# Kernel tuning notes

Hardware: AMD Instinct MI355X
Metric: run time of the kernel (lower is better)

## Reference

```python
import jax, jax.numpy as jnp
import numpy as np

B, N, K, D_IN, D, L = 8, 8192, 6, 3, 256, 5
EPS_LN = 1e-5


def layernorm(x, g, b):
    m = jnp.mean(x, axis=-1, keepdims=True)
    v = jnp.mean((x - m) ** 2, axis=-1, keepdims=True)
    return (x - m) * jax.lax.rsqrt(v + EPS_LN) * g + b


def spmm_mean(v, knn):
    # sparse adj matmul: out[j] = sum_{n: j in knn[n]} v[n], then / k
    n, k = knn.shape[-2], knn.shape[-1]
    src = jnp.repeat(jnp.arange(n), k)  # [N*K]

    def one(vb, kb):
        return jnp.zeros_like(vb).at[kb.reshape(-1)].add(vb[src])

    return jax.vmap(one)(v, knn) / (k + 1e-6)


def grf_layer(h, knn, qkv_w, out_w, out_b, hops=3):
    q, k, v = jnp.split(h @ qkv_w, 3, axis=-1)
    for _ in range(hops):
        v = spmm_mean(v, knn)
        k = spmm_mean(k, knn)
    attn = jnp.sum(q * k, axis=-1, keepdims=True)
    return (attn * v) @ out_w + out_b


def linear_attention(h, qkv_w, out_w, out_b):
    q, k, v = jnp.split(h @ qkv_w, 3, axis=-1)
    q = jax.nn.relu(q) + 1e-6
    k = jax.nn.relu(k) + 1e-6
    kv = jnp.einsum('bnd,bne->bde', k, v)
    z = 1.0 / (jnp.einsum('bnd,bd->bn', q, k.sum(axis=1)) + 1e-6)
    attn = jnp.einsum('bnd,bde,bn->bne', q, kv, z)
    return attn @ out_w + out_b


def setup_inputs() -> dict:
    key = jax.random.key(0)
    ks = jax.random.split(key, 12)
    s = 0.02
    return {
        'x': jax.random.normal(ks[0], (B, N, D_IN), jnp.float32),
        'knn': jax.random.randint(ks[1], (B, N, K), 0, N, jnp.int32),
        'emb_w': jax.random.normal(ks[2], (D_IN, D), jnp.float32) * s,
        'emb_b': jnp.zeros((D,), jnp.float32),
        'norm_g': jnp.ones((2 * L, D), jnp.float32),
        'norm_b': jnp.zeros((2 * L, D), jnp.float32),
        'grf_qkv': jax.random.normal(ks[3], (L, D, 3 * D), jnp.float32) * s,
        'grf_outw': jax.random.normal(ks[4], (L, D, D), jnp.float32) * s,
        'grf_outb': jnp.zeros((L, D), jnp.float32),
        'attn_qkv': jax.random.normal(ks[5], (L, D, 3 * D), jnp.float32) * s,
        'attn_outw': jax.random.normal(ks[6], (L, D, D), jnp.float32) * s,
        'attn_outb': jnp.zeros((L, D), jnp.float32),
        'head_w': jax.random.normal(ks[7], (D, 3), jnp.float32) * s,
        'head_b': jnp.zeros((3,), jnp.float32),
    }


def reference(x, knn, emb_w, emb_b, norm_g, norm_b, grf_qkv, grf_outw, grf_outb,
              attn_qkv, attn_outw, attn_outb, head_w, head_b):
    h = x @ emb_w + emb_b
    for i in range(L):
        h = h + grf_layer(layernorm(h, norm_g[2 * i], norm_b[2 * i]), knn,
                          grf_qkv[i], grf_outw[i], grf_outb[i])
        h = h + linear_attention(layernorm(h, norm_g[2 * i + 1], norm_b[2 * i + 1]),
                                 attn_qkv[i], attn_outw[i], attn_outb[i])
    return h @ head_w + head_b
```

## Files before the change

kernel.cpp:

```cpp
#include <hip/hip_runtime.h>

#define BB 8
#define NN 8192
#define KK 6
#define DD 256
#define LL 5
#define NE (BB*NN*KK)
#define PLANE (NN*DD)
#define INV6 (1.0f/6.000001f)

typedef unsigned short u16;
typedef __attribute__((ext_vector_type(8))) _Float16 h8;
typedef __attribute__((ext_vector_type(8))) unsigned short us8;
typedef __attribute__((ext_vector_type(4))) float f32x4;

__device__ __forceinline__ u16 f2h(float f){
  union { _Float16 h; u16 u; } c; c.h = (_Float16)f; return c.u;
}
__device__ __forceinline__ float h2f(u16 u){
  union { _Float16 h; u16 u; } c; c.u = u; return (float)c.h;
}

__device__ __forceinline__ void ldscp(const u16* g, u16* l){
  __builtin_amdgcn_global_load_lds(
      (const __attribute__((address_space(1))) void*)g,
      (__attribute__((address_space(3))) void*)l, 16, 0, 0);
}

__global__ void k_count(const int* __restrict__ knn, int* __restrict__ off){
  int e = blockIdx.x*256 + threadIdx.x;
  if(e >= NE) return;
  int b = e / (NN*KK);
  int j = knn[e];
  atomicAdd(&off[b*(NN+1) + 1 + j], 1);
}

__global__ __launch_bounds__(1024) void k_scan(int* __restrict__ offAll){
  __shared__ int lds[1024];
  __shared__ int carry_s;
  int* off = offAll + blockIdx.x*(NN+1);
  const int len = NN+1;
  int t = threadIdx.x;
  if(t==0) carry_s = 0;
  __syncthreads();
  for(int base=0; base<len; base+=1024){
    int x = (base+t < len) ? off[base+t] : 0;
    lds[t] = x; __syncthreads();
    for(int s=1; s<1024; s<<=1){
      int v = (t>=s) ? lds[t-s] : 0;
      __syncthreads();
      lds[t] += v;
      __syncthreads();
    }
    int incl = lds[t];
    int carry = carry_s;
    __syncthreads();
    if(base+t < len) off[base+t] = incl + carry;
    if(t==1023) carry_s = carry + incl;
    __syncthreads();
  }
}

__global__ void k_fill(const int* __restrict__ knn, int* __restrict__ cursor, int* __restrict__ srcE){
  int e = blockIdx.x*256 + threadIdx.x;
  if(e >= NE) return;
  int b = e / (NN*KK);
  int n = (e % (NN*KK)) / KK;
  int j = knn[e];
  int pos = atomicAdd(&cursor[b*(NN+1) + j], 1);
  srcE[(long)b*NN*KK + pos] = n;
}

__global__ __launch_bounds__(256) void k_prepw(const float* __restrict__ W, u16* __restrict__ Wt, int N){
  int n = blockIdx.x, l = blockIdx.y, k = threadIdx.x;
  float x = W[((long)l*256 + k)*N + n];
  u16 hb = f2h(x);
  Wt[(((long)l*2 + 0)*N + n)*256 + k] = hb;
  Wt[(((long)l*2 + 1)*N + n)*256 + k] = f2h(x - h2f(hb));
}

__global__ __launch_bounds__(256) void k_embed(const float* __restrict__ x, const float* __restrict__ ew,
                        const float* __restrict__ eb, float* __restrict__ h){
  int g = blockIdx.x, z = blockIdx.y, d = threadIdx.x;
  const float* xp = x + ((long)z*NN + g)*3;
  h[(long)z*PLANE + (long)g*DD + d] = xp[0]*ew[0*DD+d] + xp[1]*ew[1*DD+d] + xp[2]*ew[2*DD+d] + eb[d];
}

__global__ __launch_bounds__(256) void k_ln(const float* __restrict__ h, const float* __restrict__ g,
                     const float* __restrict__ bia, u16* __restrict__ out){
  long z = blockIdx.y;
  int row = blockIdx.x*4 + (threadIdx.x >> 6);
  int lane = threadIdx.x & 63;
  const float4 x = *(const float4*)(h + z*PLANE + (long)row*DD + lane*4);
  float s  = x.x + x.y + x.z + x.w;
  float s2 = x.x*x.x + x.y*x.y + x.z*x.z + x.w*x.w;
  for(int o=1;o<64;o<<=1){ s += __shfl_xor(s,o); s2 += __shfl_xor(s2,o); }
  float m = s*(1.0f/256.0f);
  float var = s2*(1.0f/256.0f) - m*m;
  float r = rsqrtf(var + 1e-5f);
  const float4 gu = *(const float4*)(g + lane*4);
  const float4 bu = *(const float4*)(bia + lane*4);
  ushort4 o4;
  o4.x = f2h((x.x-m)*r*gu.x + bu.x);
  o4.y = f2h((x.y-m)*r*gu.y + bu.y);
  o4.z = f2h((x.z-m)*r*gu.z + bu.z);
  o4.w = f2h((x.w-m)*r*gu.w + bu.w);
  *(ushort4*)(out + z*PLANE + (long)row*DD + lane*4) = o4;
}

template<int BM,int BN,bool ASPLIT,bool BF32,bool BSPLIT>
__global__ __launch_bounds__(256) void k_mgemm(
    const u16* __restrict__ A, long aStride, long aLoOff, int K, int kSplit,
    const void* __restrict__ Bv, long bStride, long bLoOff,
    const float* __restrict__ rowscale, long rsStride,
    const float* __restrict__ bias,
    u16* __restrict__ o0, u16* __restrict__ o1, u16* __restrict__ o2,
    long oStride, int reluMask, long oLoOff,
    float* __restrict__ accOut, long hStride)
{
  constexpr int WM = BM/2, WN = BN/2, MT = WM/16, NT = WN/16;
  constexpr int STG = BM*32*(ASPLIT?2:1) + BN*32*(BSPLIT?2:1);
  constexpr int EPI = (BM==128) ? 32*132*2 : 0;
  constexpr int SM  = (STG > EPI) ? STG : EPI;
  __shared__ __align__(16) u16 smem[SM];
  u16* Ahi = smem;
  u16* Alo = smem + BM*32;
  u16* Bhi = smem + BM*32*(ASPLIT?2:1);
  u16* Blo = Bhi + BN*32;
  float* epi = (float*)smem;

  const int t = threadIdx.x;
  const int nz = blockIdx.z;
  const long z = nz / kSplit;
  const int chunk = nz % kSplit;
  const int kLen = K / kSplit, kLo = chunk * kLen;
  const int rowTile = blockIdx.x*BM, colTile = blockIdx.y*BN;
  const int l = t & 63, w = t >> 6;
  const int wr = w >> 1, wc = w & 1;
  const int lm = l & 15, kq = l >> 4;

  f32x4 acc[MT][NT];
  #pragma unroll
  for(int mt=0;mt<MT;mt++)
    #pragma unroll
    for(int nt=0;nt<NT;nt++) acc[mt][nt] = (f32x4){0.f,0.f,0.f,0.f};

  for(int k0=kLo; k0<kLo+kLen; k0+=32){
    __syncthreads();
    {
      constexpr int NCH = BM/64;
      #pragma unroll
      for(int li=0; li<NCH; li++){
        int f = li*256 + t;
        int row = f>>2, c = (f&3)*8;
        const u16* gp = A + z*aStride + (long)(rowTile+row)*K + k0 + c;
        ldscp(gp, &Ahi[f*8]);
        if constexpr (ASPLIT) ldscp(gp + aLoOff, &Alo[f*8]);
      }
    }
    if constexpr (BF32){
      constexpr int NCH = BN/64;
      #pragma unroll
      for(int li=0; li<NCH; li++){
        int f = li*256 + t;
        int row = f>>2, c = (f&3)*8;
        const float* src = (const float*)Bv + z*bStride + (long)(colTile+row)*K + k0 + c;
        float4 v0 = ((const float4*)src)[0], v1 = ((const float4*)src)[1];
        us8 hv;
        hv[0]=f2h(v0.x); hv[1]=f2h(v0.y); hv[2]=f2h(v0.z); hv[3]=f2h(v0.w);
        hv[4]=f2h(v1.x); hv[5]=f2h(v1.y); hv[6]=f2h(v1.z); hv[7]=f2h(v1.w);
        *(us8*)&Bhi[f*8] = hv;
      }
    } else {
      constexpr int NCH = BN/64;
      #pragma unroll
      for(int li=0; li<NCH; li++){
        int f = li*256 + t;
        int row = f>>2, c = (f&3)*8;
        const u16* gp = (const u16*)Bv + z*bStride + (long)(colTile+row)*K + k0 + c;
        ldscp(gp, &Bhi[f*8]);
        if constexpr (BSPLIT) ldscp(gp + bLoOff, &Blo[f*8]);
      }
    }
    __syncthreads();
    h8 ah[MT], al[MT], bh[NT], bl[NT];
    #pragma unroll
    for(int mt=0;mt<MT;mt++){
      int idx = (wr*WM + mt*16 + lm)*32 + kq*8;
      ah[mt] = *(const h8*)&Ahi[idx];
      if constexpr (ASPLIT) al[mt] = *(const h8*)&Alo[idx];
    }
    #pragma unroll
    for(int nt=0;nt<NT;nt++){
      int idx = (wc*WN + nt*16 + lm)*32 + kq*8;
      bh[nt] = *(const h8*)&Bhi[idx];
      if constexpr (BSPLIT) bl[nt] = *(const h8*)&Blo[idx];
    }
    #pragma unroll
    for(int mt=0;mt<MT;mt++)
      #pragma unroll
      for(int nt=0;nt<NT;nt++){
        acc[mt][nt] = __builtin_amdgcn_mfma_f32_16x16x32_f16(ah[mt], bh[nt], acc[mt][nt], 0, 0, 0);
        if constexpr (BSPLIT)
          acc[mt][nt] = __builtin_amdgcn_mfma_f32_16x16x32_f16(ah[mt], bl[nt], acc[mt][nt], 0, 0, 0);
        if constexpr (ASPLIT)
          acc[mt][nt] = __builtin_amdgcn_mfma_f32_16x16x32_f16(al[mt], bh[nt], acc[mt][nt], 0, 0, 0);
      }
  }

  if constexpr (BM == 128){
    const int sec = colTile >> 8;
    u16* osec = (sec==0) ? o0 : ((sec==1) ? o1 : o2);
    const bool relu = (reluMask >> sec) & 1;
    #pragma unroll
    for(int mt=0;mt<MT;mt++){
      __syncthreads();
      #pragma unroll
      for(int r=0;r<4;r++){
        int gm = rowTile + wr*64 + mt*16 + kq*4 + r;
        float sc = rowscale ? rowscale[z*rsStride + gm] : 1.0f;
        int rl = wr*16 + kq*4 + r;
        #pragma unroll
        for(int nt=0;nt<NT;nt++)
          epi[rl*132 + wc*64 + nt*16 + lm] = acc[mt][nt][r]*sc;
      }
      __syncthreads();
      #pragma unroll
      for(int ss=0;ss<2;ss++){
        int s = ss*256 + t;
        int rl = s >> 4, sc8 = (s & 15)*8;
        int gm2 = rowTile + (rl>>4)*64 + mt*16 + (rl & 15);
        float v[8];
        #pragma unroll
        for(int j=0;j<8;j++) v[j] = epi[rl*132 + sc8 + j];
        if(bias){
          const float* bp = bias + colTile + sc8;
          #pragma unroll
          for(int j=0;j<8;j++) v[j] += bp[j];
        }
        if(accOut){
          float* hp = accOut + z*hStride + (long)gm2*256 + colTile + sc8;
          float4 h0 = ((float4*)hp)[0], h1 = ((float4*)hp)[1];
          h0.x += v[0]; h0.y += v[1]; h0.z += v[2]; h0.w += v[3];
          h1.x += v[4]; h1.y += v[5]; h1.z += v[6]; h1.w += v[7];
          ((float4*)hp)[0] = h0; ((float4*)hp)[1] = h1;
        } else {
          us8 o8;
          #pragma unroll
          for(int j=0;j<8;j++){
            float vv = v[j];
            if(relu) vv = fmaxf(vv, 0.f) + 1e-6f;
            o8[j] = f2h(vv);
          }
          *(us8*)(osec + z*oStride + (long)gm2*256 + ((colTile + sc8) & 255)) = o8;
        }
      }
    }
  } else {
    #pragma unroll
    for(int mt=0;mt<MT;mt++){
      #pragma unroll
      for(int r=0;r<4;r++){
        int gm = rowTile + wr*WM + mt*16 + kq*4 + r;
        float sc = rowscale ? rowscale[z*rsStride + gm] : 1.0f;
        if(accOut){
          float* hp = accOut + z*hStride + (long)gm*256;
          if(kSplit > 1){
            #pragma unroll
            for(int nt=0;nt<NT;nt++){
              int gc = colTile + wc*WN + nt*16 + lm;
              atomicAdd(&hp[gc], acc[mt][nt][r]);
            }
          } else {
            #pragma unroll
            for(int nt=0;nt<NT;nt++){
              int gc = colTile + wc*WN + nt*16 + lm;
              hp[gc] += acc[mt][nt][r]*sc + (bias ? bias[gc] : 0.f);
            }
          }
        } else {
          #pragma unroll
          for(int nt=0;nt<NT;nt++){
            int gc = colTile + wc*WN + nt*16 + lm;
            int sec = gc >> 8;
            u16* o = (sec==0) ? o0 : ((sec==1) ? o1 : o2);
            float val = acc[mt][nt][r]*sc + (bias ? bias[gc] : 0.f);
            if((reluMask >> sec) & 1) val = fmaxf(val, 0.f) + 1e-6f;
            if(sec==0 && oLoOff){
              u16* oo = o0 + 2*z*oStride + (long)gm*256 + (gc & 255);
              u16 hb = f2h(val);
              oo[0] = hb;
              oo[oLoOff] = f2h(val - h2f(hb));
            } else {
              o[z*oStride + (long)gm*256 + (gc & 255)] = f2h(val);
            }
          }
        }
      }
    }
  }
}

__global__ __launch_bounds__(256) void k_fusedout(
    const u16* __restrict__ A, const u16* __restrict__ B, long bStride, long bLoOff,
    const float* __restrict__ rowscale, const float* __restrict__ bias,
    float* __restrict__ h,
    const float* __restrict__ lnG, const float* __restrict__ lnB,
    u16* __restrict__ Lout)
{
  __shared__ __align__(16) u16 smem[16384];
  u16* Bh = smem;
  u16* Bl = smem + 8192;
  float* epi = (float*)smem;

  const int t = threadIdx.x;
  const long z = blockIdx.z;
  const int rowTile = blockIdx.x*32;
  const int l = t & 63, w = t >> 6;
  const int wr = w >> 1, wc = w & 1;
  const int lm = l & 15, kq = l >> 4;
  const u16* Ab = A + z*PLANE;
  const u16* Bb = B + z*bStride;

  f32x4 acc[8];
  #pragma unroll
  for(int nt=0;nt<8;nt++) acc[nt] = (f32x4){0.f,0.f,0.f,0.f};

  h8 areg[8];
  {
    const u16* arow = Ab + (long)(rowTile + wr*16 + lm)*256 + kq*8;
    #pragma unroll
    for(int kk=0;kk<8;kk++) areg[kk] = *(const h8*)(arow + kk*32);
  }

  #pragma unroll
  for(int kk=0; kk<8; ++kk){
    __syncthreads();
    #pragma unroll
    for(int li=0; li<4; li++){
      int f = li*256 + t;
      int row = f>>2, c = (f&3)*8;
      const u16* gp = Bb + (long)row*256 + kk*32 + c;
      ldscp(gp, &Bh[f*8]);
      ldscp(gp + bLoOff, &Bl[f*8]);
    }
    __syncthreads();
    #pragma unroll
    for(int nt=0;nt<8;nt++){
      int idx = (wc*128 + nt*16 + lm)*32 + kq*8;
      const h8 bhf = *(const h8*)&Bh[idx];
      const h8 blf = *(const h8*)&Bl[idx];
      acc[nt] = __builtin_amdgcn_mfma_f32_16x16x32_f16(areg[kk], bhf, acc[nt], 0, 0, 0);
      acc[nt] = __builtin_amdgcn_mfma_f32_16x16x32_f16(areg[kk], blf, acc[nt], 0, 0, 0);
    }
  }

  #pragma unroll
  for(int p=0;p<2;p++){
    __syncthreads();
    if(wr == p){
      #pragma unroll
      for(int r=0;r<4;r++){
        int rl = kq*4 + r;
        int gm = rowTile + p*16 + rl;
        float sc = rowscale ? rowscale[z*NN + gm] : 1.0f;
        #pragma unroll
        for(int nt=0;nt<8;nt++)
          epi[rl*260 + wc*128 + nt*16 + lm] = acc[nt][r]*sc;
      }
    }
    __syncthreads();
    #pragma unroll
    for(int ss=0;ss<4;ss++){
      int s = ss*256 + t;
      int rl = s >> 6;
      int c4 = (s & 63)*4;
      int gm = rowTile + p*16 + rl;
      float4 e = *(float4*)&epi[rl*260 + c4];
      float4 x;
      x.x = e.x + bias[c4+0];
      x.y = e.y + bias[c4+1];
      x.z = e.z + bias[c4+2];
      x.w = e.w + bias[c4+3];
      float* hp = h + z*PLANE + (long)gm*256 + c4;
      float4 h0 = *(float4*)hp;
      x.x += h0.x; x.y += h0.y; x.z += h0.z; x.w += h0.w;
      *(float4*)hp = x;
      if(lnG){
        float sA = x.x + x.y + x.z + x.w;
        float s2 = x.x*x.x + x.y*x.y + x.z*x.z + x.w*x.w;
        for(int o=1;o<64;o<<=1){ sA += __shfl_xor(sA,o); s2 += __shfl_xor(s2,o); }
        float m = sA*(1.0f/256.0f);
        float var = s2*(1.0f/256.0f) - m*m;
        float rr = rsqrtf(var + 1e-5f);
        const float4 gu = *(const float4*)(lnG + c4);
        const float4 bu = *(const float4*)(lnB + c4);
        ushort4 o4;
        o4.x = f2h((x.x-m)*rr*gu.x + bu.x);
        o4.y = f2h((x.y-m)*rr*gu.y + bu.y);
        o4.z = f2h((x.z-m)*rr*gu.z + bu.z);
        o4.w = f2h((x.w-m)*rr*gu.w + bu.w);
        *(ushort4*)(Lout + z*PLANE + (long)gm*256 + c4) = o4;
      }
    }
  }
}

template<int MODE>
__global__ __launch_bounds__(256) void k_spmm2(
    const u16* __restrict__ kin, const u16* __restrict__ vin,
    const int* __restrict__ offB, const int* __restrict__ srcB,
    u16* __restrict__ kout, u16* __restrict__ vout,
    const u16* __restrict__ q, float* __restrict__ rs){
  long z = blockIdx.x;
  const int* off = offB + z*(NN+1);
  const int* sE  = srcB + z*(long)NN*KK;

  if constexpr (MODE == 0){
    const u16* kp = kin + z*PLANE;
    const u16* vp = vin + z*PLANE;
    int row = blockIdx.y*16 + (threadIdx.x >> 4);
    int d8 = blockIdx.z*128 + (threadIdx.x & 15)*8;
    int s0 = off[row], s1 = off[row+1];
    float ak[8], av[8];
    #pragma unroll
    for(int j=0;j<8;j++){ ak[j]=0.f; av[j]=0.f; }
    int e = s0;
    for(; e+1 < s1; e += 2){
      int n0 = sE[e], n1 = sE[e+1];
      us8 k0 = *(const us8*)(kp + (long)n0*DD + d8);
      us8 k1 = *(const us8*)(kp + (long)n1*DD + d8);
      us8 v0 = *(const us8*)(vp + (long)n0*DD + d8);
      us8 v1 = *(const us8*)(vp + (long)n1*DD + d8);
      #pragma unroll
      for(int j=0;j<8;j++){
        ak[j] += h2f(k0[j]) + h2f(k1[j]);
        av[j] += h2f(v0[j]) + h2f(v1[j]);
      }
    }
    if(e < s1){
      int n0 = sE[e];
      us8 k0 = *(const us8*)(kp + (long)n0*DD + d8);
      us8 v0 = *(const us8*)(vp + (long)n0*DD + d8);
      #pragma unroll
      for(int j=0;j<8;j++){ ak[j] += h2f(k0[j]); av[j] += h2f(v0[j]); }
    }
    us8 ok, ov;
    #pragma unroll
    for(int j=0;j<8;j++){ ok[j] = f2h(ak[j]*INV6); ov[j] = f2h(av[j]*INV6); }
    *(us8*)(kout + z*PLANE + (long)row*DD + d8) = ok;
    *(us8*)(vout + z*PLANE + (long)row*DD + d8) = ov;
  } else {
    if(blockIdx.z == 0){
      const u16* kp = kin + z*PLANE;
      int row = blockIdx.y*8 + (threadIdx.x >> 5);
      int l32 = threadIdx.x & 31;
      int d8 = l32*8;
      int s0 = off[row], s1 = off[row+1];
      float ak[8];
      #pragma unroll
      for(int j=0;j<8;j++) ak[j]=0.f;
      int e = s0;
      for(; e+1 < s1; e += 2){
        int n0 = sE[e], n1 = sE[e+1];
        us8 k0 = *(const us8*)(kp + (long)n0*DD + d8);
        us8 k1 = *(const us8*)(kp + (long)n1*DD + d8);
        #pragma unroll
        for(int j=0;j<8;j++) ak[j] += h2f(k0[j]) + h2f(k1[j]);
      }
      if(e < s1){
        int n0 = sE[e];
        us8 k0 = *(const us8*)(kp + (long)n0*DD + d8);
        #pragma unroll
        for(int j=0;j<8;j++) ak[j] += h2f(k0[j]);
      }
      us8 qv = *(const us8*)(q + z*PLANE + (long)row*DD + d8);
      float s = 0.f;
      #pragma unroll
      for(int j=0;j<8;j++) s += h2f(qv[j]) * ak[j];
      for(int o=1;o<32;o<<=1) s += __shfl_xor(s,o);
      if(l32==0) rs[z*NN + row] = s*INV6;
    } else {
      const u16* vp = vin + z*PLANE;
      int row = (blockIdx.y & 511)*16 + (threadIdx.x >> 4);
      int d8 = (blockIdx.y >> 9)*128 + (threadIdx.x & 15)*8;
      int s0 = off[row], s1 = off[row+1];
      float av[8];
      #pragma unroll
      for(int j=0;j<8;j++) av[j]=0.f;
      int e = s0;
      for(; e+1 < s1; e += 2){
        int n0 = sE[e], n1 = sE[e+1];
        us8 v0 = *(const us8*)(vp + (long)n0*DD + d8);
        us8 v1 = *(const us8*)(vp + (long)n1*DD + d8);
        #pragma unroll
        for(int j=0;j<8;j++) av[j] += h2f(v0[j]) + h2f(v1[j]);
      }
      if(e < s1){
        int n0 = sE[e];
        us8 v0 = *(const us8*)(vp + (long)n0*DD + d8);
        #pragma unroll
        for(int j=0;j<8;j++) av[j] += h2f(v0[j]);
      }
      us8 ov;
      #pragma unroll
      for(int j=0;j<8;j++) ov[j] = f2h(av[j]*INV6);
      *(us8*)(vout + z*PLANE + (long)row*DD + d8) = ov;
    }
  }
}

__global__ __launch_bounds__(256) void k_zcalc(const u16* __restrict__ q, const float* __restrict__ ksum,
                        float* __restrict__ rs){
  long z = blockIdx.y;
  int row = blockIdx.x*4 + (threadIdx.x >> 6);
  int lane = threadIdx.x & 63;
  ushort4 qv = *(const ushort4*)(q + z*PLANE + (long)row*DD + lane*4);
  const float4 c = *(const float4*)(ksum + z*DD + lane*4);
  float s = h2f(qv.x)*c.x + h2f(qv.y)*c.y + h2f(qv.z)*c.z + h2f(qv.w)*c.w;
  for(int o=1;o<64;o<<=1) s += __shfl_xor(s,o);
  if(lane==0) rs[z*NN + row] = 1.0f / (s + 1e-6f);
}

__global__ __launch_bounds__(256) void k_transp2(
    const u16* __restrict__ in0, u16* __restrict__ out0,
    const u16* __restrict__ in1, u16* __restrict__ out1){
  __shared__ u16 tile[64][72];
  int zz = blockIdx.z;
  long z = zz >> 1;
  const u16* ip = ((zz & 1) ? in1 : in0) + z*PLANE;
  u16* op = ((zz & 1) ? out1 : out0) + z*PLANE;
  int r0 = blockIdx.x*64, c0 = blockIdx.y*64;
  int t = threadIdx.x;
  {
    int r = t>>2, cg = (t&3)*16;
    *(us8*)&tile[r][cg]   = *(const us8*)(ip + (long)(r0+r)*DD + c0 + cg);
    *(us8*)&tile[r][cg+8] = *(const us8*)(ip + (long)(r0+r)*DD + c0 + cg + 8);
  }
  __syncthreads();
  {
    int c = t>>2, rg = t&3;
    us8 a, b;
    #pragma unroll
    for(int j=0;j<8;j++){ a[j] = tile[rg*16+j][c]; b[j] = tile[rg*16+8+j][c]; }
    u16* dst = op + (long)(c0+c)*NN + r0 + rg*16;
    *(us8*)dst = a; *(us8*)(dst+8) = b;
  }
}

__global__ __launch_bounds__(256) void k_ksum(const u16* __restrict__ kT, float* __restrict__ ksum){
  long z = blockIdx.y;
  int d = blockIdx.x;
  const u16* p = kT + z*PLANE + (long)d*NN;
  float s = 0.f;
  for(int i=threadIdx.x*8; i<NN; i+=2048){
    us8 a = *(const us8*)(p+i);
    #pragma unroll
    for(int j=0;j<8;j++) s += h2f(a[j]);
  }
  for(int o=1;o<64;o<<=1) s += __shfl_xor(s,o);
  __shared__ float ws4[4];
  int w = threadIdx.x >> 6;
  if((threadIdx.x & 63)==0) ws4[w] = s;
  __syncthreads();
  if(threadIdx.x==0) ksum[z*DD + d] = ws4[0]+ws4[1]+ws4[2]+ws4[3];
}

__global__ __launch_bounds__(256) void k_head(const float* __restrict__ h, const float* __restrict__ hw,
                       const float* __restrict__ hb, float* __restrict__ out){
  long z = blockIdx.y;
  int row = blockIdx.x*4 + (threadIdx.x >> 6);
  int lane = threadIdx.x & 63;
  const float4 x = *(const float4*)(h + z*PLANE + (long)row*DD + lane*4);
  int d0 = lane*4;
  float a0 = x.x*hw[(d0+0)*3+0] + x.y*hw[(d0+1)*3+0] + x.z*hw[(d0+2)*3+0] + x.w*hw[(d0+3)*3+0];
  float a1 = x.x*hw[(d0+0)*3+1] + x.y*hw[(d0+1)*3+1] + x.z*hw[(d0+2)*3+1] + x.w*hw[(d0+3)*3+1];
  float a2 = x.x*hw[(d0+0)*3+2] + x.y*hw[(d0+1)*3+2] + x.z*hw[(d0+2)*3+2] + x.w*hw[(d0+3)*3+2];
  for(int o=1;o<64;o<<=1){
    a0 += __shfl_xor(a0,o); a1 += __shfl_xor(a1,o); a2 += __shfl_xor(a2,o);
  }
  if(lane==0){
    float* op = out + (z*NN + row)*3;
    op[0] = a0 + hb[0];
    op[1] = a1 + hb[1];
    op[2] = a2 + hb[2];
  }
}

struct Carve {
  float *h; u16 *L,*Q,*Bp,*Cp,*T;
  float *kvf; u16 *w2t;
  float *ksum,*rs;
  int *off,*cursor,*srcE;
  u16 *wt_gqkv,*wt_aqkv,*wt_gout,*wt_aout;
  size_t total;
};

static Carve carve(char* base, int C){
  Carve c;
  size_t cur = 0;
  auto bump = [&](size_t bytes)->char*{
    char* p = base ? base + cur : (char*)0;
    cur += (bytes + 255) & ~(size_t)255;
    return p;
  };
  c.h    = (float*)bump((size_t)C*PLANE*4);
  c.L    = (u16*)bump((size_t)C*PLANE*2);
  c.Q    = (u16*)bump((size_t)C*PLANE*2);
  c.Bp   = (u16*)bump((size_t)C*PLANE*2);
  c.Cp   = (u16*)bump((size_t)C*PLANE*2);
  c.T    = (u16*)bump((size_t)C*PLANE*2);
  c.kvf  = (float*)bump((size_t)C*DD*DD*4);
  c.w2t  = (u16*)bump((size_t)C*2*DD*DD*2);
  c.ksum = (float*)bump((size_t)C*DD*4);
  c.rs   = (float*)bump((size_t)C*NN*4);
  c.off  = (int*)bump((size_t)BB*(NN+1)*4);
  c.cursor=(int*)bump((size_t)BB*(NN+1)*4);
  c.srcE = (int*)bump((size_t)NE*4);
  c.wt_gqkv = (u16*)bump((size_t)LL*2*768*256*2);
  c.wt_aqkv = (u16*)bump((size_t)LL*2*768*256*2);
  c.wt_gout = (u16*)bump((size_t)LL*2*256*256*2);
  c.wt_aout = (u16*)bump((size_t)LL*2*256*256*2);
  c.total = cur;
  return c;
}

extern "C" void kernel_launch(void* const* d_in, const int* in_sizes, int n_in,
                              void* d_out, int out_size, void* d_ws, size_t ws_size,
                              hipStream_t stream)
{
  const float* x        = (const float*)d_in[0];
  const int*   knn      = (const int*)d_in[1];
  const float* emb_w    = (const float*)d_in[2];
  const float* emb_b    = (const float*)d_in[3];
  const float* norm_g   = (const float*)d_in[4];
  const float* norm_b   = (const float*)d_in[5];
  const float* grf_qkv  = (const float*)d_in[6];
  const float* grf_outw = (const float*)d_in[7];
  const float* grf_outb = (const float*)d_in[8];
  const float* attn_qkv = (const float*)d_in[9];
  const float* attn_outw= (const float*)d_in[10];
  const float* attn_outb= (const float*)d_in[11];
  const float* head_w   = (const float*)d_in[12];
  const float* head_b   = (const float*)d_in[13];
  float* out = (float*)d_out;

  int C = 1;
  for(int cc=BB; cc>=1; cc>>=1){ if(carve(nullptr, cc).total <= ws_size){ C = cc; break; } }
  Carve ws = carve((char*)d_ws, C);

  k_prepw<<<dim3(768, LL), 256, 0, stream>>>(grf_qkv,  ws.wt_gqkv, 768);
  k_prepw<<<dim3(768, LL), 256, 0, stream>>>(attn_qkv, ws.wt_aqkv, 768);
  k_prepw<<<dim3(256, LL), 256, 0, stream>>>(grf_outw, ws.wt_gout, 256);
  k_prepw<<<dim3(256, LL), 256, 0, stream>>>(attn_outw,ws.wt_aout, 256);

  hipMemsetAsync(ws.off, 0, (size_t)BB*(NN+1)*sizeof(int), stream);
  k_count<<<dim3((NE+255)/256), 256, 0, stream>>>(knn, ws.off);
  k_scan<<<dim3(BB), 1024, 0, stream>>>(ws.off);
  hipMemcpyAsync(ws.cursor, ws.off, (size_t)BB*(NN+1)*sizeof(int), hipMemcpyDeviceToDevice, stream);
  k_fill<<<dim3((NE+255)/256), 256, 0, stream>>>(knn, ws.cursor, ws.srcE);

  const long PL = PLANE;
  for(int b0=0; b0<BB; b0+=C){
    const int* offB  = ws.off  + (long)b0*(NN+1);
    const int* srcB  = ws.srcE + (long)b0*NN*KK;

    k_embed<<<dim3(NN, C), 256, 0, stream>>>(x + (long)b0*NN*3, emb_w, emb_b, ws.h);
    k_ln<<<dim3(NN/4, C), 256, 0, stream>>>(ws.h, norm_g, norm_b, ws.L);

    for(int i=0; i<LL; i++){
      k_mgemm<128,128,false,false,true><<<dim3(64, 6, C), 256, 0, stream>>>(
          ws.L, PL, 0, 256, 1,
          ws.wt_gqkv + (long)i*2*768*256, 0, (long)768*256,
          nullptr, 0, nullptr,
          ws.Q, ws.Bp, ws.Cp, PL, 0, 0, nullptr, 0);
      k_spmm2<0><<<dim3(C, NN/16, 2), 256, 0, stream>>>(ws.Bp, ws.Cp, offB, srcB, ws.L, ws.T, nullptr, nullptr);
      k_spmm2<0><<<dim3(C, NN/16, 2), 256, 0, stream>>>(ws.L,  ws.T,  offB, srcB, ws.Bp, ws.Cp, nullptr, nullptr);
      k_spmm2<1><<<dim3(C, NN/8, 2), 256, 0, stream>>>(ws.Bp, ws.Cp, offB, srcB, nullptr, ws.T, ws.Q, ws.rs);
      k_fusedout<<<dim3(NN/32, 1, C), 256, 0, stream>>>(
          ws.T, ws.wt_gout + (long)i*2*256*256, 0, (long)256*256,
          ws.rs, grf_outb + (long)i*DD, ws.h,
          norm_g + (2*i+1)*DD, norm_b + (2*i+1)*DD, ws.L);

      k_mgemm<128,128,false,false,true><<<dim3(64, 6, C), 256, 0, stream>>>(
          ws.L, PL, 0, 256, 1,
          ws.wt_aqkv + (long)i*2*768*256, 0, (long)768*256,
          nullptr, 0, nullptr,
          ws.Q, ws.Bp, ws.Cp, PL, 3 , 0, nullptr, 0);
      k_transp2<<<dim3(NN/64, DD/64, 2*C), 256, 0, stream>>>(ws.Bp, ws.L, ws.Cp, ws.T);
      k_ksum<<<dim3(DD, C), 256, 0, stream>>>(ws.L, ws.ksum);
      hipMemsetAsync(ws.kvf, 0, (size_t)C*DD*DD*sizeof(float), stream);
      k_mgemm<64,64,false,false,false><<<dim3(4, 4, C*8), 256, 0, stream>>>(
          ws.L, PL, 0, NN, 8,
          ws.T, PL, 0,
          nullptr, 0, nullptr,
          nullptr, nullptr, nullptr, 0, 0, 0, ws.kvf, (long)DD*DD);
      k_mgemm<64,64,true,true,false><<<dim3(4, 4, C), 256, 0, stream>>>(
          ws.wt_aout + (long)i*2*256*256, 0, (long)256*256, 256, 1,
          ws.kvf, (long)DD*DD, 0,
          nullptr, 0, nullptr,
          ws.w2t, nullptr, nullptr, (long)DD*DD, 0, (long)DD*DD,
          nullptr, 0);
      k_zcalc<<<dim3(NN/4, C), 256, 0, stream>>>(ws.Q, ws.ksum, ws.rs);
      const float* g2 = (i==LL-1) ? nullptr : norm_g + (2*i+2)*DD;
      const float* b2 = (i==LL-1) ? nullptr : norm_b + (2*i+2)*DD;
      k_fusedout<<<dim3(NN/32, 1, C), 256, 0, stream>>>(
          ws.Q, ws.w2t, 2L*DD*DD, (long)DD*DD,
          ws.rs, attn_outb + (long)i*DD, ws.h,
          g2, b2, ws.L);
    }

    k_head<<<dim3(NN/4, C), 256, 0, stream>>>(ws.h, head_w, head_b, out + (long)b0*NN*3);
  }
}
```

Measured before the change: 2.586 ms.

## Double-buffer LDS staging in the f16 MFMA GEMM main loop

For the non-fp32-B GEMM variants, the K loop now uses two LDS buffers. The next K-slice is issued with async global-to-LDS copies before the MFMAs on the current slice, so load latency can overlap compute and one barrier per iteration is dropped. The fp32-B path keeps the original single-buffer loop. Shared memory per block doubles for these variants, which may lower occupancy. Correctness depends on the barrier at the end of each iteration also waiting for the outstanding LDS DMA writes.

```diff
diff --git a/kernel.cpp b/kernel.cpp
--- a/kernel.cpp
+++ b/kernel.cpp
@@ -119,14 +119,11 @@
     float* __restrict__ accOut, long hStride)
 {
   constexpr int WM = BM/2, WN = BN/2, MT = WM/16, NT = WN/16;
-  constexpr int STG = BM*32*(ASPLIT?2:1) + BN*32*(BSPLIT?2:1);
+  constexpr int STG1 = BM*32*(ASPLIT?2:1) + BN*32*(BSPLIT?2:1);
+  constexpr int STGT = BF32 ? STG1 : 2*STG1;
   constexpr int EPI = (BM==128) ? 32*132*2 : 0;
-  constexpr int SM  = (STG > EPI) ? STG : EPI;
+  constexpr int SM  = (STGT > EPI) ? STGT : EPI;
   __shared__ __align__(16) u16 smem[SM];
-  u16* Ahi = smem;
-  u16* Alo = smem + BM*32;
-  u16* Bhi = smem + BM*32*(ASPLIT?2:1);
-  u16* Blo = Bhi + BN*32;
   float* epi = (float*)smem;
 
   const int t = threadIdx.x;
@@ -145,67 +142,126 @@
     #pragma unroll
     for(int nt=0;nt<NT;nt++) acc[mt][nt] = (f32x4){0.f,0.f,0.f,0.f};
 
-  for(int k0=kLo; k0<kLo+kLen; k0+=32){
+  if constexpr (!BF32){
+    auto stageAB = [&](int buf, int k0){
+      u16* Ahi_ = smem + (size_t)buf*STG1;
+      u16* Alo_ = Ahi_ + BM*32;
+      u16* Bhi_ = Ahi_ + BM*32*(ASPLIT?2:1);
+      u16* Blo_ = Bhi_ + BN*32;
+      {
+        constexpr int NCH = BM/64;
+        #pragma unroll
+        for(int li=0; li<NCH; li++){
+          int f = li*256 + t;
+          int row = f>>2, c = (f&3)*8;
+          const u16* gp = A + z*aStride + (long)(rowTile+row)*K + k0 + c;
+          ldscp(gp, &Ahi_[f*8]);
+          if constexpr (ASPLIT) ldscp(gp + aLoOff, &Alo_[f*8]);
+        }
+      }
+      {
+        constexpr int NCH = BN/64;
+        #pragma unroll
+        for(int li=0; li<NCH; li++){
+          int f = li*256 + t;
+          int row = f>>2, c = (f&3)*8;
+          const u16* gp = (const u16*)Bv + z*bStride + (long)(colTile+row)*K + k0 + c;
+          ldscp(gp, &Bhi_[f*8]);
+          if constexpr (BSPLIT) ldscp(gp + bLoOff, &Blo_[f*8]);
+        }
+      }
+    };
+
+    const int nsteps = kLen >> 5;
+    stageAB(0, kLo);
     __syncthreads();
-    {
-      constexpr int NCH = BM/64;
-      #pragma unroll
-      for(int li=0; li<NCH; li++){
-        int f = li*256 + t;
-        int row = f>>2, c = (f&3)*8;
-        const u16* gp = A + z*aStride + (long)(rowTile+row)*K + k0 + c;
-        ldscp(gp, &Ahi[f*8]);
-        if constexpr (ASPLIT) ldscp(gp + aLoOff, &Alo[f*8]);
-      }
-    }
-    if constexpr (BF32){
-      constexpr int NCH = BN/64;
-      #pragma unroll
-      for(int li=0; li<NCH; li++){
-        int f = li*256 + t;
-        int row = f>>2, c = (f&3)*8;
-        const float* src = (const float*)Bv + z*bStride + (long)(colTile+row)*K + k0 + c;
-        float4 v0 = ((const float4*)src)[0], v1 = ((const float4*)src)[1];
-        us8 hv;
-        hv[0]=f2h(v0.x); hv[1]=f2h(v0.y); hv[2]=f2h(v0.z); hv[3]=f2h(v0.w);
-        hv[4]=f2h(v1.x); hv[5]=f2h(v1.y); hv[6]=f2h(v1.z); hv[7]=f2h(v1.w);
-        *(us8*)&Bhi[f*8] = hv;
-      }
-    } else {
-      constexpr int NCH = BN/64;
-      #pragma unroll
-      for(int li=0; li<NCH; li++){
-        int f = li*256 + t;
-        int row = f>>2, c = (f&3)*8;
-        const u16* gp = (const u16*)Bv + z*bStride + (long)(colTile+row)*K + k0 + c;
-        ldscp(gp, &Bhi[f*8]);
-        if constexpr (BSPLIT) ldscp(gp + bLoOff, &Blo[f*8]);
-      }
-    }
-    __syncthreads();
-    h8 ah[MT], al[MT], bh[NT], bl[NT];
-    #pragma unroll
-    for(int mt=0;mt<MT;mt++){
-      int idx = (wr*WM + mt*16 + lm)*32 + kq*8;
-      ah[mt] = *(const h8*)&Ahi[idx];
-      if constexpr (ASPLIT) al[mt] = *(const h8*)&Alo[idx];
-    }
-    #pragma unroll
-    for(int nt=0;nt<NT;nt++){
-      int idx = (wc*WN + nt*16 + lm)*32 + kq*8;
-      bh[nt] = *(const h8*)&Bhi[idx];
-      if constexpr (BSPLIT) bl[nt] = *(const h8*)&Blo[idx];
-    }
-    #pragma unroll
-    for(int mt=0;mt<MT;mt++)
+    int cur = 0;
+    for(int ks=0; ks<nsteps; ++ks){
+      if(ks+1 < nsteps) stageAB(cur^1, kLo + ((ks+1)<<5));
+      const u16* Ahi_ = smem + (size_t)cur*STG1;
+      const u16* Alo_ = Ahi_ + BM*32;
+      const u16* Bhi_ = Ahi_ + BM*32*(ASPLIT?2:1);
+      const u16* Blo_ = Bhi_ + BN*32;
+      h8 ah[MT], al[MT], bh[NT], bl[NT];
+      #pragma unroll
+      for(int mt=0;mt<MT;mt++){
+        int idx = (wr*WM + mt*16 + lm)*32 + kq*8;
+        ah[mt] = *(const h8*)&Ahi_[idx];
+        if constexpr (ASPLIT) al[mt] = *(const h8*)&Alo_[idx];
+      }
       #pragma unroll
       for(int nt=0;nt<NT;nt++){
-        acc[mt][nt] = __builtin_amdgcn_mfma_f32_16x16x32_f16(ah[mt], bh[nt], acc[mt][nt], 0, 0, 0);
-        if constexpr (BSPLIT)
-          acc[mt][nt] = __builtin_amdgcn_mfma_f32_16x16x32_f16(ah[mt], bl[nt], acc[mt][nt], 0, 0, 0);
-        if constexpr (ASPLIT)
-          acc[mt][nt] = __builtin_amdgcn_mfma_f32_16x16x32_f16(al[mt], bh[nt], acc[mt][nt], 0, 0, 0);
-      }
+        int idx = (wc*WN + nt*16 + lm)*32 + kq*8;
+        bh[nt] = *(const h8*)&Bhi_[idx];
+        if constexpr (BSPLIT) bl[nt] = *(const h8*)&Blo_[idx];
+      }
+      #pragma unroll
+      for(int mt=0;mt<MT;mt++)
+        #pragma unroll
+        for(int nt=0;nt<NT;nt++){
+          acc[mt][nt] = __builtin_amdgcn_mfma_f32_16x16x32_f16(ah[mt], bh[nt], acc[mt][nt], 0, 0, 0);
+          if constexpr (BSPLIT)
+            acc[mt][nt] = __builtin_amdgcn_mfma_f32_16x16x32_f16(ah[mt], bl[nt], acc[mt][nt], 0, 0, 0);
+          if constexpr (ASPLIT)
+            acc[mt][nt] = __builtin_amdgcn_mfma_f32_16x16x32_f16(al[mt], bh[nt], acc[mt][nt], 0, 0, 0);
+        }
+      __syncthreads();
+      cur ^= 1;
+    }
+  } else {
+    u16* Ahi = smem;
+    u16* Alo = smem + BM*32;
+    u16* Bhi = smem + BM*32*(ASPLIT?2:1);
+    u16* Blo = Bhi + BN*32;
+    for(int k0=kLo; k0<kLo+kLen; k0+=32){
+      __syncthreads();
+      {
+        constexpr int NCH = BM/64;
+        #pragma unroll
+        for(int li=0; li<NCH; li++){
+          int f = li*256 + t;
+          int row = f>>2, c = (f&3)*8;
+          const u16* gp = A + z*aStride + (long)(rowTile+row)*K + k0 + c;
+          ldscp(gp, &Ahi[f*8]);
+          if constexpr (ASPLIT) ldscp(gp + aLoOff, &Alo[f*8]);
+        }
+      }
+      {
+        constexpr int NCH = BN/64;
+        #pragma unroll
+        for(int li=0; li<NCH; li++){
+          int f = li*256 + t;
+          int row = f>>2, c = (f&3)*8;
+          const float* src = (const float*)Bv + z*bStride + (long)(colTile+row)*K + k0 + c;
+          float4 v0 = ((const float4*)src)[0], v1 = ((const float4*)src)[1];
+          us8 hv;
+          hv[0]=f2h(v0.x); hv[1]=f2h(v0.y); hv[2]=f2h(v0.z); hv[3]=f2h(v0.w);
+          hv[4]=f2h(v1.x); hv[5]=f2h(v1.y); hv[6]=f2h(v1.z); hv[7]=f2h(v1.w);
+          *(us8*)&Bhi[f*8] = hv;
+        }
+      }
+      __syncthreads();
+      h8 ah[MT], al[MT], bh[NT];
+      #pragma unroll
+      for(int mt=0;mt<MT;mt++){
+        int idx = (wr*WM + mt*16 + lm)*32 + kq*8;
+        ah[mt] = *(const h8*)&Ahi[idx];
+        if constexpr (ASPLIT) al[mt] = *(const h8*)&Alo[idx];
+      }
+      #pragma unroll
+      for(int nt=0;nt<NT;nt++){
+        int idx = (wc*WN + nt*16 + lm)*32 + kq*8;
+        bh[nt] = *(const h8*)&Bhi[idx];
+      }
+      #pragma unroll
+      for(int mt=0;mt<MT;mt++)
+        #pragma unroll
+        for(int nt=0;nt<NT;nt++){
+          acc[mt][nt] = __builtin_amdgcn_mfma_f32_16x16x32_f16(ah[mt], bh[nt], acc[mt][nt], 0, 0, 0);
+          if constexpr (ASPLIT)
+            acc[mt][nt] = __builtin_amdgcn_mfma_f32_16x16x32_f16(al[mt], bh[nt], acc[mt][nt], 0, 0, 0);
+        }
+    }
   }
 
   if constexpr (BM == 128){
```

Result: no change. 2.555 ms (-1.2%).
